# Optimization experiments

Measured on AMD Instinct MI355X. Metric: run time of the kernel, lower is better.

## Reference

```python
import jax, jax.numpy as jnp
import numpy as np

D_MODEL = 1024
N_HEADS = 16
HEAD_DIM = D_MODEL // N_HEADS


def setup_inputs() -> dict:
    key = jax.random.key(0)
    ks = jax.random.split(key, 5)
    B, T = 2, 2048
    x = jax.random.normal(ks[0], (B, T, D_MODEL), dtype=jnp.float32)
    s_in = 1.0 / np.sqrt(D_MODEL)
    W_qkv = jax.random.normal(ks[1], (D_MODEL, 3 * D_MODEL), dtype=jnp.float32) * s_in
    b_qkv = jnp.zeros((3 * D_MODEL,), dtype=jnp.float32)
    W_out = jax.random.normal(ks[2], (D_MODEL, D_MODEL), dtype=jnp.float32) * s_in
    b_out = jnp.zeros((D_MODEL,), dtype=jnp.float32)
    return {"x": x, "W_qkv": W_qkv, "b_qkv": b_qkv, "W_out": W_out, "b_out": b_out}


def reference(x, W_qkv, b_qkv, W_out, b_out):
    B, T, C = x.shape
    qkv = x @ W_qkv + b_qkv  # (B, T, 3C)
    q, k, v = jnp.split(qkv, 3, axis=-1)
    # (B, H, T, Dh)
    q = q.reshape(B, T, N_HEADS, HEAD_DIM).transpose(0, 2, 1, 3)
    k = k.reshape(B, T, N_HEADS, HEAD_DIM).transpose(0, 2, 1, 3)
    v = v.reshape(B, T, N_HEADS, HEAD_DIM).transpose(0, 2, 1, 3)
    scale = 1.0 / jnp.sqrt(jnp.asarray(HEAD_DIM, dtype=x.dtype))
    scores = jnp.einsum('bhqd,bhkd->bhqk', q, k) * scale  # (B, H, T, T)
    causal = jnp.tril(jnp.ones((T, T), dtype=bool))
    scores = jnp.where(causal[None, None], scores, jnp.asarray(-jnp.inf, dtype=scores.dtype))
    attn = jax.nn.softmax(scores, axis=-1)
    out = jnp.einsum('bhqk,bhkd->bhqd', attn, v)  # (B, H, T, Dh)
    out = out.transpose(0, 2, 1, 3).reshape(B, T, C)
    return out @ W_out + b_out
```

## Files before the change

### kernel.cpp

```cpp
#include <hip/hip_runtime.h>
#include <hip/hip_bf16.h>
#include <stdint.h>

typedef __bf16 bf16;
typedef __bf16 bf16x4 __attribute__((ext_vector_type(4)));
typedef __bf16 bf16x8 __attribute__((ext_vector_type(8)));
typedef float  f32x4  __attribute__((ext_vector_type(4)));

#define D_MODEL 1024
#define N_HEADS 16
#define HEAD_DIM 64
#define SEQ 2048
#define BATCH 2
#define LOG2E 1.4426950408889634f
#define NEG_SENT -3.0e4f
#define CAP 24.0f

__device__ __forceinline__ bf16x8 ld8(const bf16* p) { return *(const bf16x8*)p; }

__device__ __forceinline__ void async16(const bf16* g, bf16* l) {
  __builtin_amdgcn_global_load_lds(
      (const __attribute__((address_space(1))) void*)g,
      (__attribute__((address_space(3))) void*)l, 16, 0, 0);
}

__global__ __launch_bounds__(256)
void prep(const float* __restrict__ x, bf16* __restrict__ x16,
          const float* __restrict__ Wqkv, bf16* __restrict__ Wqkv_t,
          const float* __restrict__ Wout, bf16* __restrict__ Wout_t) {
  __shared__ float tile[32][33];
  const int blk = blockIdx.x, tid = threadIdx.x;
  if (blk < 4096) {
    int i = (blk * 256 + tid) * 4;
    float4 v = *(const float4*)&x[i];
    bf16 o[4] = {(bf16)v.x, (bf16)v.y, (bf16)v.z, (bf16)v.w};
    *(uint2*)&x16[i] = *(uint2*)o;
    return;
  }
  const float* in; bf16* out; int R, C, c0, r0;
  if (blk < 7168) {
    int b = blk - 4096;
    in = Wqkv; out = Wqkv_t; R = 1024; C = 3072;
    c0 = (b % 96) * 32; r0 = (b / 96) * 32;
  } else {
    int b = blk - 7168;
    in = Wout; out = Wout_t; R = 1024; C = 1024;
    c0 = (b % 32) * 32; r0 = (b / 32) * 32;
  }
  const int tx = tid & 31, ty = tid >> 5;
  #pragma unroll
  for (int i = 0; i < 32; i += 8)
    tile[ty + i][tx] = in[(size_t)(r0 + ty + i) * C + c0 + tx];
  __syncthreads();
  #pragma unroll
  for (int i = 0; i < 32; i += 8)
    out[(size_t)(c0 + ty + i) * R + r0 + tx] = (bf16)tile[tx][ty + i];
}

__global__ __launch_bounds__(256)
void gemm_bt(const bf16* __restrict__ A, const bf16* __restrict__ Bt,
             const float* __restrict__ bias, float* __restrict__ outf,
             bf16* __restrict__ Qp, bf16* __restrict__ Kp, bf16* __restrict__ Vtp,
             int N, int mode) {
  __shared__ __align__(16) bf16 shA[128 * 32];
  __shared__ __align__(16) bf16 shB[128 * 32];
  const int tid  = threadIdx.x;
  const int bm0  = blockIdx.y * 128, bn0 = blockIdx.x * 128;
  const int wave = tid >> 6, lane = tid & 63;
  const int quad = lane >> 4, l16 = lane & 15;
  const int wm = (wave >> 1) * 64, wn = (wave & 1) * 64;

  const int c_lo  = tid;
  const int row_lo = c_lo >> 2,  col_lo = (c_lo & 3) << 3;
  const int c_hi  = tid + 256;
  const int row_hi = c_hi >> 2,  col_hi = (c_hi & 3) << 3;
  const int cb_lo = (wave * 64) * 8;
  const int cb_hi = (256 + wave * 64) * 8;

  f32x4 acc[4][4];
  #pragma unroll
  for (int i = 0; i < 4; i++)
    #pragma unroll
    for (int j = 0; j < 4; j++)
      acc[i][j] = (f32x4){0.f, 0.f, 0.f, 0.f};

  for (int k0 = 0; k0 < 1024; k0 += 32) {
    async16(&A[(size_t)(bm0 + row_lo) * 1024 + k0 + col_lo], &shA[cb_lo]);
    async16(&A[(size_t)(bm0 + row_hi) * 1024 + k0 + col_hi], &shA[cb_hi]);
    async16(&Bt[(size_t)(bn0 + row_lo) * 1024 + k0 + col_lo], &shB[cb_lo]);
    async16(&Bt[(size_t)(bn0 + row_hi) * 1024 + k0 + col_hi], &shB[cb_hi]);
    __syncthreads();
    bf16x8 af[4], bg[4];
    #pragma unroll
    for (int i = 0; i < 4; i++)
      af[i] = ld8(&shA[(wm + i * 16 + l16) * 32 + quad * 8]);
    #pragma unroll
    for (int j = 0; j < 4; j++)
      bg[j] = ld8(&shB[(wn + j * 16 + l16) * 32 + quad * 8]);
    #pragma unroll
    for (int i = 0; i < 4; i++)
      #pragma unroll
      for (int j = 0; j < 4; j++)
        acc[i][j] = __builtin_amdgcn_mfma_f32_16x16x32_bf16(af[i], bg[j], acc[i][j], 0, 0, 0);
    __syncthreads();
  }

  #pragma unroll
  for (int i = 0; i < 4; i++) {
    #pragma unroll
    for (int j = 0; j < 4; j++) {
      int gn = bn0 + wn + j * 16 + l16;
      float bv = bias[gn];
      int gm0 = bm0 + wm + i * 16 + quad * 4;
      if (mode == 1) {
        #pragma unroll
        for (int r = 0; r < 4; r++)
          outf[(size_t)(gm0 + r) * N + gn] = acc[i][j][r] + bv;
      } else {
        int which = gn >> 10, rem = gn & 1023;
        int h = rem >> 6, d = rem & 63;
        int b = gm0 >> 11, t0 = gm0 & 2047;
        int bh = b * N_HEADS + h;
        if (which == 2) {
          bf16x4 vv = {(bf16)(acc[i][j][0] + bv), (bf16)(acc[i][j][1] + bv),
                       (bf16)(acc[i][j][2] + bv), (bf16)(acc[i][j][3] + bv)};
          *(bf16x4*)&Vtp[((size_t)bh * 64 + d) * SEQ + t0] = vv;
        } else {
          bf16* dst = (which == 0) ? Qp : Kp;
          #pragma unroll
          for (int r = 0; r < 4; r++)
            dst[((size_t)bh * SEQ + t0 + r) * 64 + d] = (bf16)(acc[i][j][r] + bv);
        }
      }
    }
  }
}

__global__ __launch_bounds__(256)
void attn_k(const bf16* __restrict__ Qp, const bf16* __restrict__ Kp,
            const bf16* __restrict__ Vtp, bf16* __restrict__ Obuf) {
  __shared__ __align__(16) bf16 shK[128 * 64];
  __shared__ __align__(16) bf16 shV[64 * 128];
  __shared__ __align__(16) bf16 shPT[4][16 * 72];
  const int tid  = threadIdx.x;
  const int wave = tid >> 6, lane = tid & 63;
  const int quad = lane >> 4, l16 = lane & 15;
  const int bh = blockIdx.y, bx = blockIdx.x;
  const int qb = (bx & 1) ? (31 - (bx >> 1)) : (bx >> 1);
  const int qw0 = qb * 64 + wave * 16;

  const bf16* Qbh = Qp  + (size_t)bh * SEQ * 64;
  const bf16* Kbh = Kp  + (size_t)bh * SEQ * 64;
  const bf16* Vbh = Vtp + (size_t)bh * 64 * SEQ;

  bf16x8 aQ[2];
  #pragma unroll
  for (int p = 0; p < 2; p++)
    aQ[p] = ld8(&Qbh[(size_t)(qw0 + l16) * 64 + p * 32 + quad * 8]);

  f32x4 o[4];
  #pragma unroll
  for (int j = 0; j < 4; j++) o[j] = (f32x4){0.f, 0.f, 0.f, 0.f};
  f32x4 lacc = (f32x4){0.f, 0.f, 0.f, 0.f};
  const int qlane = qw0 + l16;
  const int xq = l16 & 7;

  const float SC = 0.125f * LOG2E;
  const int NT = qb >> 1;
  bf16* PT = shPT[wave];

  for (int kt = 0; kt <= NT; kt++) {
    const int kbase = kt * 128;
    __syncthreads();
    #pragma unroll
    for (int s = 0; s < 4; s++) {
      int id = tid + s * 256;
      int kr = id >> 3, kc = id & 7;
      async16(&Kbh[(size_t)(kbase + kr) * 64 + (kc ^ (kr & 7)) * 8], &shK[id * 8]);
    }
    #pragma unroll
    for (int s = 0; s < 4; s++) {
      int id = tid + s * 256;
      int vd = id >> 4, vc = id & 15;
      int svc = (vc & 8) | ((vc & 7) ^ (vd & 7));
      async16(&Vbh[(size_t)vd * SEQ + kbase + svc * 8], &shV[id * 8]);
    }
    __syncthreads();

    #pragma unroll
    for (int h = 0; h < 2; h++) {
      const int hb = kbase + h * 64;
      if (hb > qw0 + 15) continue;

      f32x4 st[4];
      #pragma unroll
      for (int c = 0; c < 4; c++) {
        int kr0 = h * 64 + c * 16 + l16;
        bf16x8 kf0 = ld8(&shK[kr0 * 64 + ((quad    ) ^ xq) * 8]);
        bf16x8 kf1 = ld8(&shK[kr0 * 64 + ((quad + 4) ^ xq) * 8]);
        f32x4 acc = (f32x4){0.f, 0.f, 0.f, 0.f};
        acc = __builtin_amdgcn_mfma_f32_16x16x32_bf16(kf0, aQ[0], acc, 0, 0, 0);
        acc = __builtin_amdgcn_mfma_f32_16x16x32_bf16(kf1, aQ[1], acc, 0, 0, 0);
        st[c] = acc;
      }

      if (hb + 63 > qw0) {
        #pragma unroll
        for (int c = 0; c < 4; c++)
          #pragma unroll
          for (int r = 0; r < 4; r++) {
            int key = hb + c * 16 + quad * 4 + r;
            if (key > qlane) st[c][r] = NEG_SENT;
          }
      }

      #pragma unroll
      for (int c = 0; c < 4; c++) {
        #pragma unroll
        for (int r = 0; r < 4; r++)
          st[c][r] = exp2f(__builtin_fmaf(st[c][r], SC, -CAP));
        lacc += st[c];
      }

      if (h == 1)
        asm volatile("s_waitcnt lgkmcnt(0)" ::: "memory");
      #pragma unroll
      for (int c = 0; c < 4; c++) {
        bf16x4 pv = {(bf16)st[c][0], (bf16)st[c][1], (bf16)st[c][2], (bf16)st[c][3]};
        *(bf16x4*)&PT[l16 * 72 + c * 16 + quad * 4] = pv;
      }
      asm volatile("s_waitcnt lgkmcnt(0)" ::: "memory");
      bf16x8 bP0 = ld8(&PT[l16 * 72 + quad * 8]);
      bf16x8 bP1 = ld8(&PT[l16 * 72 + 32 + quad * 8]);

      #pragma unroll
      for (int j = 0; j < 4; j++) {
        int d = j * 16 + l16;
        bf16x8 v0 = ld8(&shV[d * 128 + ((h * 8) | ((quad    ) ^ xq)) * 8]);
        bf16x8 v1 = ld8(&shV[d * 128 + ((h * 8) | ((quad + 4) ^ xq)) * 8]);
        o[j] = __builtin_amdgcn_mfma_f32_16x16x32_bf16(v0, bP0, o[j], 0, 0, 0);
        o[j] = __builtin_amdgcn_mfma_f32_16x16x32_bf16(v1, bP1, o[j], 0, 0, 0);
      }
    }
  }

  float lrow = (lacc[0] + lacc[1]) + (lacc[2] + lacc[3]);
  lrow += __shfl_xor(lrow, 16, 64);
  lrow += __shfl_xor(lrow, 32, 64);

  const int b = bh >> 4, h = bh & 15;
  {
    float inv = 1.0f / lrow;
    int t = qw0 + l16;
    size_t base = ((size_t)(b * SEQ + t)) * D_MODEL + h * 64;
    #pragma unroll
    for (int j = 0; j < 4; j++) {
      bf16x4 ov = {(bf16)(o[j][0] * inv), (bf16)(o[j][1] * inv),
                   (bf16)(o[j][2] * inv), (bf16)(o[j][3] * inv)};
      *(bf16x4*)&Obuf[base + j * 16 + quad * 4] = ov;
    }
  }
}

extern "C" void kernel_launch(void* const* d_in, const int* in_sizes, int n_in,
                              void* d_out, int out_size, void* d_ws, size_t ws_size,
                              hipStream_t stream) {
  const float* x    = (const float*)d_in[0];
  const float* Wqkv = (const float*)d_in[1];
  const float* bqkv = (const float*)d_in[2];
  const float* Wout = (const float*)d_in[3];
  const float* bout = (const float*)d_in[4];
  float* out = (float*)d_out;

  char* ws = (char*)d_ws;
  bf16* x16    = (bf16*)(ws);
  bf16* Wqkv_t = (bf16*)(ws + 8388608);
  bf16* Wout_t = (bf16*)(ws + 14680064);
  bf16* Qp     = (bf16*)(ws + 16777216);
  bf16* Kp     = (bf16*)(ws + 25165824);
  bf16* Vtp    = (bf16*)(ws + 33554432);
  bf16* Obuf   = x16;

  prep<<<8192, 256, 0, stream>>>(x, x16, Wqkv, Wqkv_t, Wout, Wout_t);

  gemm_bt<<<dim3(3072 / 128, 4096 / 128), 256, 0, stream>>>(
      x16, Wqkv_t, bqkv, nullptr, Qp, Kp, Vtp, 3072, 0);

  attn_k<<<dim3(32, BATCH * N_HEADS), 256, 0, stream>>>(Qp, Kp, Vtp, Obuf);

  gemm_bt<<<dim3(1024 / 128, 4096 / 128), 256, 0, stream>>>(
      Obuf, Wout_t, bout, out, nullptr, nullptr, nullptr, 1024, 1);
}
```

Measured before the change: 218.8 us.

## Load K and V fragments directly from global memory instead of LDS staging

Drops the shared-memory staging of K and V tiles and the two block-wide barriers per key tile. Each wave now loads its K and V MFMA fragments straight from global memory into registers, and the MFMA sections are wrapped in s_setprio raises. The aim is to remove barrier stalls and LDS traffic, at the cost of redundant global/L2 reads, since all four waves fetch the same K/V, and uncoalesced 16-byte loads with more register pressure.

```diff
diff --git a/kernel.cpp b/kernel.cpp
--- a/kernel.cpp
+++ b/kernel.cpp
@@ -139,8 +139,6 @@
 __global__ __launch_bounds__(256)
 void attn_k(const bf16* __restrict__ Qp, const bf16* __restrict__ Kp,
             const bf16* __restrict__ Vtp, bf16* __restrict__ Obuf) {
-  __shared__ __align__(16) bf16 shK[128 * 64];
-  __shared__ __align__(16) bf16 shV[64 * 128];
   __shared__ __align__(16) bf16 shPT[4][16 * 72];
   const int tid  = threadIdx.x;
   const int wave = tid >> 6, lane = tid & 63;
@@ -163,45 +161,42 @@
   for (int j = 0; j < 4; j++) o[j] = (f32x4){0.f, 0.f, 0.f, 0.f};
   f32x4 lacc = (f32x4){0.f, 0.f, 0.f, 0.f};
   const int qlane = qw0 + l16;
-  const int xq = l16 & 7;
 
   const float SC = 0.125f * LOG2E;
   const int NT = qb >> 1;
   bf16* PT = shPT[wave];
 
   for (int kt = 0; kt <= NT; kt++) {
-    const int kbase = kt * 128;
-    __syncthreads();
-    #pragma unroll
-    for (int s = 0; s < 4; s++) {
-      int id = tid + s * 256;
-      int kr = id >> 3, kc = id & 7;
-      async16(&Kbh[(size_t)(kbase + kr) * 64 + (kc ^ (kr & 7)) * 8], &shK[id * 8]);
-    }
-    #pragma unroll
-    for (int s = 0; s < 4; s++) {
-      int id = tid + s * 256;
-      int vd = id >> 4, vc = id & 15;
-      int svc = (vc & 8) | ((vc & 7) ^ (vd & 7));
-      async16(&Vbh[(size_t)vd * SEQ + kbase + svc * 8], &shV[id * 8]);
-    }
-    __syncthreads();
-
     #pragma unroll
     for (int h = 0; h < 2; h++) {
-      const int hb = kbase + h * 64;
+      const int hb = kt * 128 + h * 64;
       if (hb > qw0 + 15) continue;
 
+      bf16x8 kf[4][2];
+      #pragma unroll
+      for (int c = 0; c < 4; c++) {
+        const bf16* kr = &Kbh[(size_t)(hb + c * 16 + l16) * 64 + quad * 8];
+        kf[c][0] = ld8(kr);
+        kf[c][1] = ld8(kr + 32);
+      }
+
       f32x4 st[4];
-      #pragma unroll
-      for (int c = 0; c < 4; c++) {
-        int kr0 = h * 64 + c * 16 + l16;
-        bf16x8 kf0 = ld8(&shK[kr0 * 64 + ((quad    ) ^ xq) * 8]);
-        bf16x8 kf1 = ld8(&shK[kr0 * 64 + ((quad + 4) ^ xq) * 8]);
+      __builtin_amdgcn_s_setprio(1);
+      #pragma unroll
+      for (int c = 0; c < 4; c++) {
         f32x4 acc = (f32x4){0.f, 0.f, 0.f, 0.f};
-        acc = __builtin_amdgcn_mfma_f32_16x16x32_bf16(kf0, aQ[0], acc, 0, 0, 0);
-        acc = __builtin_amdgcn_mfma_f32_16x16x32_bf16(kf1, aQ[1], acc, 0, 0, 0);
+        acc = __builtin_amdgcn_mfma_f32_16x16x32_bf16(kf[c][0], aQ[0], acc, 0, 0, 0);
+        acc = __builtin_amdgcn_mfma_f32_16x16x32_bf16(kf[c][1], aQ[1], acc, 0, 0, 0);
         st[c] = acc;
+      }
+      __builtin_amdgcn_s_setprio(0);
+
+      bf16x8 vf[4][2];
+      #pragma unroll
+      for (int j = 0; j < 4; j++) {
+        const bf16* vr = &Vbh[(size_t)(j * 16 + l16) * SEQ + hb + quad * 8];
+        vf[j][0] = ld8(vr);
+        vf[j][1] = ld8(vr + 32);
       }
 
       if (hb + 63 > qw0) {
@@ -222,8 +217,7 @@
         lacc += st[c];
       }
 
-      if (h == 1)
-        asm volatile("s_waitcnt lgkmcnt(0)" ::: "memory");
+      asm volatile("s_waitcnt lgkmcnt(0)" ::: "memory");
       #pragma unroll
       for (int c = 0; c < 4; c++) {
         bf16x4 pv = {(bf16)st[c][0], (bf16)st[c][1], (bf16)st[c][2], (bf16)st[c][3]};
@@ -233,14 +227,13 @@
       bf16x8 bP0 = ld8(&PT[l16 * 72 + quad * 8]);
       bf16x8 bP1 = ld8(&PT[l16 * 72 + 32 + quad * 8]);
 
+      __builtin_amdgcn_s_setprio(1);
       #pragma unroll
       for (int j = 0; j < 4; j++) {
-        int d = j * 16 + l16;
-        bf16x8 v0 = ld8(&shV[d * 128 + ((h * 8) | ((quad    ) ^ xq)) * 8]);
-        bf16x8 v1 = ld8(&shV[d * 128 + ((h * 8) | ((quad + 4) ^ xq)) * 8]);
-        o[j] = __builtin_amdgcn_mfma_f32_16x16x32_bf16(v0, bP0, o[j], 0, 0, 0);
-        o[j] = __builtin_amdgcn_mfma_f32_16x16x32_bf16(v1, bP1, o[j], 0, 0, 0);
-      }
+        o[j] = __builtin_amdgcn_mfma_f32_16x16x32_bf16(vf[j][0], bP0, o[j], 0, 0, 0);
+        o[j] = __builtin_amdgcn_mfma_f32_16x16x32_bf16(vf[j][1], bP1, o[j], 0, 0, 0);
+      }
+      __builtin_amdgcn_s_setprio(0);
     }
   }
 
```

New measurement: 368.8 us. +68.5%, slower.

## Double-buffer 64-key K/V tiles in attention with async prefetch of next tile

Applied to the files above, without the earlier changes.

The attention kernel switches from single-buffered 128-key K/V tiles, loaded between two barriers, to double-buffered 64-key tiles. The next tile is issued with async global-to-LDS loads while the current one is computed, which hides load latency and cuts barriers per key block. Causal masking now applies only on the diagonal tile, and the per-wave half-tile skip is gone. In exchange, smaller tiles mean more loop iterations and one barrier per 64 keys.

```diff
diff --git a/kernel.cpp b/kernel.cpp
--- a/kernel.cpp
+++ b/kernel.cpp
@@ -139,8 +139,8 @@
 __global__ __launch_bounds__(256)
 void attn_k(const bf16* __restrict__ Qp, const bf16* __restrict__ Kp,
             const bf16* __restrict__ Vtp, bf16* __restrict__ Obuf) {
-  __shared__ __align__(16) bf16 shK[128 * 64];
-  __shared__ __align__(16) bf16 shV[64 * 128];
+  __shared__ __align__(16) bf16 shK[2][64 * 64];
+  __shared__ __align__(16) bf16 shV[2][64 * 64];
   __shared__ __align__(16) bf16 shPT[4][16 * 72];
   const int tid  = threadIdx.x;
   const int wave = tid >> 6, lane = tid & 63;
@@ -153,6 +153,8 @@
   const bf16* Kbh = Kp  + (size_t)bh * SEQ * 64;
   const bf16* Vbh = Vtp + (size_t)bh * 64 * SEQ;
 
+  const int kr_s = tid >> 3, kc_s = tid & 7;
+
   bf16x8 aQ[2];
   #pragma unroll
   for (int p = 0; p < 2; p++)
@@ -166,82 +168,96 @@
   const int xq = l16 & 7;
 
   const float SC = 0.125f * LOG2E;
-  const int NT = qb >> 1;
   bf16* PT = shPT[wave];
 
-  for (int kt = 0; kt <= NT; kt++) {
-    const int kbase = kt * 128;
+  {
+    #pragma unroll
+    for (int i = 0; i < 2; i++) {
+      int kr = kr_s + i * 32;
+      async16(&Kbh[(size_t)kr * 64 + (kc_s ^ (kr & 7)) * 8],
+              &shK[0][(kr * 8 + kc_s) * 8]);
+    }
+    #pragma unroll
+    for (int i = 0; i < 2; i++) {
+      int vd = kr_s + i * 32;
+      async16(&Vbh[(size_t)vd * SEQ + (kc_s ^ (vd & 7)) * 8],
+              &shV[0][(vd * 8 + kc_s) * 8]);
+    }
+  }
+  __syncthreads();
+
+  int cur = 0;
+  for (int s = 0; s <= qb; s++) {
+    if (s < qb) {
+      const int kb1 = (s + 1) * 64;
+      #pragma unroll
+      for (int i = 0; i < 2; i++) {
+        int kr = kr_s + i * 32;
+        async16(&Kbh[(size_t)(kb1 + kr) * 64 + (kc_s ^ (kr & 7)) * 8],
+                &shK[cur ^ 1][(kr * 8 + kc_s) * 8]);
+      }
+      #pragma unroll
+      for (int i = 0; i < 2; i++) {
+        int vd = kr_s + i * 32;
+        async16(&Vbh[(size_t)vd * SEQ + kb1 + (kc_s ^ (vd & 7)) * 8],
+                &shV[cur ^ 1][(vd * 8 + kc_s) * 8]);
+      }
+    }
+
+    const bf16* Kb = shK[cur];
+    const bf16* Vb = shV[cur];
+    const int hb = s * 64;
+
+    f32x4 st[4];
+    #pragma unroll
+    for (int c = 0; c < 4; c++) {
+      int kr0 = c * 16 + l16;
+      bf16x8 kf0 = ld8(&Kb[kr0 * 64 + ((quad    ) ^ xq) * 8]);
+      bf16x8 kf1 = ld8(&Kb[kr0 * 64 + ((quad + 4) ^ xq) * 8]);
+      f32x4 acc = (f32x4){0.f, 0.f, 0.f, 0.f};
+      acc = __builtin_amdgcn_mfma_f32_16x16x32_bf16(kf0, aQ[0], acc, 0, 0, 0);
+      acc = __builtin_amdgcn_mfma_f32_16x16x32_bf16(kf1, aQ[1], acc, 0, 0, 0);
+      st[c] = acc;
+    }
+
+    if (s == qb) {
+      #pragma unroll
+      for (int c = 0; c < 4; c++)
+        #pragma unroll
+        for (int r = 0; r < 4; r++) {
+          int key = hb + c * 16 + quad * 4 + r;
+          if (key > qlane) st[c][r] = NEG_SENT;
+        }
+    }
+
+    #pragma unroll
+    for (int c = 0; c < 4; c++) {
+      #pragma unroll
+      for (int r = 0; r < 4; r++)
+        st[c][r] = exp2f(__builtin_fmaf(st[c][r], SC, -CAP));
+      lacc += st[c];
+    }
+
+    #pragma unroll
+    for (int c = 0; c < 4; c++) {
+      bf16x4 pv = {(bf16)st[c][0], (bf16)st[c][1], (bf16)st[c][2], (bf16)st[c][3]};
+      *(bf16x4*)&PT[l16 * 72 + c * 16 + quad * 4] = pv;
+    }
+    asm volatile("s_waitcnt lgkmcnt(0)" ::: "memory");
+    bf16x8 bP0 = ld8(&PT[l16 * 72 + quad * 8]);
+    bf16x8 bP1 = ld8(&PT[l16 * 72 + 32 + quad * 8]);
+
+    #pragma unroll
+    for (int j = 0; j < 4; j++) {
+      int d = j * 16 + l16;
+      bf16x8 v0 = ld8(&Vb[d * 64 + ((quad    ) ^ xq) * 8]);
+      bf16x8 v1 = ld8(&Vb[d * 64 + ((quad + 4) ^ xq) * 8]);
+      o[j] = __builtin_amdgcn_mfma_f32_16x16x32_bf16(v0, bP0, o[j], 0, 0, 0);
+      o[j] = __builtin_amdgcn_mfma_f32_16x16x32_bf16(v1, bP1, o[j], 0, 0, 0);
+    }
+
     __syncthreads();
-    #pragma unroll
-    for (int s = 0; s < 4; s++) {
-      int id = tid + s * 256;
-      int kr = id >> 3, kc = id & 7;
-      async16(&Kbh[(size_t)(kbase + kr) * 64 + (kc ^ (kr & 7)) * 8], &shK[id * 8]);
-    }
-    #pragma unroll
-    for (int s = 0; s < 4; s++) {
-      int id = tid + s * 256;
-      int vd = id >> 4, vc = id & 15;
-      int svc = (vc & 8) | ((vc & 7) ^ (vd & 7));
-      async16(&Vbh[(size_t)vd * SEQ + kbase + svc * 8], &shV[id * 8]);
-    }
-    __syncthreads();
-
-    #pragma unroll
-    for (int h = 0; h < 2; h++) {
-      const int hb = kbase + h * 64;
-      if (hb > qw0 + 15) continue;
-
-      f32x4 st[4];
-      #pragma unroll
-      for (int c = 0; c < 4; c++) {
-        int kr0 = h * 64 + c * 16 + l16;
-        bf16x8 kf0 = ld8(&shK[kr0 * 64 + ((quad    ) ^ xq) * 8]);
-        bf16x8 kf1 = ld8(&shK[kr0 * 64 + ((quad + 4) ^ xq) * 8]);
-        f32x4 acc = (f32x4){0.f, 0.f, 0.f, 0.f};
-        acc = __builtin_amdgcn_mfma_f32_16x16x32_bf16(kf0, aQ[0], acc, 0, 0, 0);
-        acc = __builtin_amdgcn_mfma_f32_16x16x32_bf16(kf1, aQ[1], acc, 0, 0, 0);
-        st[c] = acc;
-      }
-
-      if (hb + 63 > qw0) {
-        #pragma unroll
-        for (int c = 0; c < 4; c++)
-          #pragma unroll
-          for (int r = 0; r < 4; r++) {
-            int key = hb + c * 16 + quad * 4 + r;
-            if (key > qlane) st[c][r] = NEG_SENT;
-          }
-      }
-
-      #pragma unroll
-      for (int c = 0; c < 4; c++) {
-        #pragma unroll
-        for (int r = 0; r < 4; r++)
-          st[c][r] = exp2f(__builtin_fmaf(st[c][r], SC, -CAP));
-        lacc += st[c];
-      }
-
-      if (h == 1)
-        asm volatile("s_waitcnt lgkmcnt(0)" ::: "memory");
-      #pragma unroll
-      for (int c = 0; c < 4; c++) {
-        bf16x4 pv = {(bf16)st[c][0], (bf16)st[c][1], (bf16)st[c][2], (bf16)st[c][3]};
-        *(bf16x4*)&PT[l16 * 72 + c * 16 + quad * 4] = pv;
-      }
-      asm volatile("s_waitcnt lgkmcnt(0)" ::: "memory");
-      bf16x8 bP0 = ld8(&PT[l16 * 72 + quad * 8]);
-      bf16x8 bP1 = ld8(&PT[l16 * 72 + 32 + quad * 8]);
-
-      #pragma unroll
-      for (int j = 0; j < 4; j++) {
-        int d = j * 16 + l16;
-        bf16x8 v0 = ld8(&shV[d * 128 + ((h * 8) | ((quad    ) ^ xq)) * 8]);
-        bf16x8 v1 = ld8(&shV[d * 128 + ((h * 8) | ((quad + 4) ^ xq)) * 8]);
-        o[j] = __builtin_amdgcn_mfma_f32_16x16x32_bf16(v0, bP0, o[j], 0, 0, 0);
-        o[j] = __builtin_amdgcn_mfma_f32_16x16x32_bf16(v1, bP1, o[j], 0, 0, 0);
-      }
-    }
+    cur ^= 1;
   }
 
   float lrow = (lacc[0] + lacc[1]) + (lacc[2] + lacc[3]);
```

Result: no change. 220.0 us (+0.5%).
